# Optimization experiments

Hardware: AMD Instinct MI355X
Metric: run time of the kernel (lower is better)

The kernel has to match this reference:

```python
import jax, jax.numpy as jnp
import numpy as np

B = 2048          # args.batch_size
NPOS = 3          # n_positives
D = 128           # feature dim
TEMP = 0.1        # temperature
N_NEG = 4096      # args.n_negative
WEIGHT = 1.0      # args.multi_pos_weight
N = B * (1 + NPOS)  # total rows in z = 8192


def setup_inputs() -> dict:
    key = jax.random.key(0)
    k1, k2 = jax.random.split(key)
    return {
        "x": jax.random.normal(k1, (NPOS * B, D), dtype=jnp.float32),
        "x_pair": jax.random.normal(k2, (B, D), dtype=jnp.float32),
    }


def _l2n(a):
    return a / jnp.linalg.norm(a, axis=-1, keepdims=True)


def reference(x, x_pair):
    # z = cat(x, x_pair); full cosine-similarity matrix scaled by temperature
    z = jnp.concatenate([x, x_pair], axis=0)          # [N, D]
    zn = _l2n(z)
    sim = (zn @ zn.T) / TEMP                          # [N, N]

    # positive loss: per-row cosine(p, x_pair) for each of NPOS chunks of x
    xn = _l2n(x.reshape(NPOS, B, D))                  # [NPOS, B, D]
    pn = _l2n(x_pair)                                 # [B, D]
    pos = jnp.sum(xn * pn[None, :, :], axis=-1) / TEMP  # [NPOS, B]
    loss_pos = WEIGHT * pos.mean(axis=1).sum() / NPOS

    # drop diagonal: row i keeps all columns j != i (row-major, matches boolean-mask reshape)
    cols = jnp.arange(N - 1)[None, :]
    cols = cols + (cols >= jnp.arange(N)[:, None])    # [N, N-1]
    neg = jnp.take_along_axis(sim, cols, axis=1)      # [N, N-1]

    # random negative subsampling: per-row random permutation, keep first N_NEG
    u = jax.random.uniform(jax.random.key(42), (N, N - 1))
    perm = jnp.argsort(u, axis=1)[:, :N_NEG]          # [N, N_NEG]
    neg = jnp.take_along_axis(neg, perm, axis=1)

    loss_neg = jax.nn.logsumexp(neg, axis=1).mean()
    return loss_neg - loss_pos
```

## Files before the change

kernel.cpp:

```cpp
#include <hip/hip_runtime.h>
#include <hip/hip_bf16.h>
#include <stdint.h>

#define NTOT 8192
#define DD   128
#define BB   2048
#define NX   6144
#define LOG_SUB_FRAC (-0.6930251f)
#define SQRT10 3.16227766017f

typedef __attribute__((ext_vector_type(4))) float floatx4;

#define GLOBAL_AS(p) ((const __attribute__((address_space(1))) void*)(p))
#define LDS_AS(p)    ((__attribute__((address_space(3))) void*)(p))

template <int CTRL>
__device__ __forceinline__ float dpp_add(float s) {
  return s + __int_as_float(
      __builtin_amdgcn_update_dpp(0, __float_as_int(s), CTRL, 0xF, 0xF, true));
}
__device__ __forceinline__ float row16_sum(float s) {
  s = dpp_add<0xB1>(s);
  s = dpp_add<0x4E>(s);
  s = dpp_add<0x124>(s);
  s = dpp_add<0x128>(s);
  return s;
}

__global__ __launch_bounds__(256) void mp_norm(const float* __restrict__ x,
                                               const float* __restrict__ xp,
                                               uint8_t* __restrict__ znb8,
                                               float* __restrict__ pos,
                                               float* __restrict__ rowtotals) {
  const int z = blockIdx.x * 256 + threadIdx.x;
  if (z < NTOT) rowtotals[z] = 0.f;

  const int row  = blockIdx.x * 4 + (threadIdx.x >> 6);
  const int lane = threadIdx.x & 63;
  const bool isx = row < NX;
  const float* src = isx ? (x + (size_t)row * DD) : (xp + (size_t)(row - NX) * DD);
  float2 v = ((const float2*)src)[lane];
  float ss = v.x * v.x + v.y * v.y;

  float ssp = 0.f, d = 0.f;
  if (isx) {
    const int b = row & (BB - 1);
    float2 p = ((const float2*)(xp + (size_t)b * DD))[lane];
    ssp = p.x * p.x + p.y * p.y;
    d = v.x * p.x + v.y * p.y;
  }
  ss  = row16_sum(ss);  ss  += __shfl_xor(ss, 16, 64);  ss  += __shfl_xor(ss, 32, 64);
  if (isx) {
    ssp = row16_sum(ssp); ssp += __shfl_xor(ssp, 16, 64); ssp += __shfl_xor(ssp, 32, 64);
    d   = row16_sum(d);   d   += __shfl_xor(d, 16, 64);   d   += __shfl_xor(d, 32, 64);
  }
  const float rn = rsqrtf(ss);
  const float rns = rn * SQRT10;
  const int pk = __builtin_amdgcn_cvt_pk_fp8_f32(v.x * rns, v.y * rns, 0, false);
  *(uint16_t*)(znb8 + (size_t)row * DD + lane * 2) = (uint16_t)(pk & 0xffff);
  if (isx && lane == 0) pos[row] = d * rn * rsqrtf(ssp);
}

__global__ __launch_bounds__(256, 4) void mp_simexp(const uint8_t* __restrict__ znb8,
                                                    float* __restrict__ rowtotals) {
  __shared__ uint8_t Asmem[128 * 128];
  __shared__ uint8_t Bsmem[128 * 128];

  const int t = blockIdx.x;
  int bi = (int)((129.0f - sqrtf(16641.0f - 8.0f * (float)t)) * 0.5f);
  #define FCUM(r) ((r) * 64 - ((r) * ((r) - 1)) / 2)
  while (bi > 0 && FCUM(bi) > t) --bi;
  while (FCUM(bi + 1) <= t) ++bi;
  const int bj = bi + (t - FCUM(bi));
  const bool diag = (bi == bj);

  const int tid  = threadIdx.x;
  const int wave = tid >> 6, lane = tid & 63;
  const int lhi = lane >> 4, llo = lane & 15;

  const uint8_t* gA = znb8 + (size_t)bi * 128 * DD;
  const uint8_t* gB = znb8 + (size_t)bj * 128 * DD;

  #pragma unroll
  for (int tc = 0; tc < 4; ++tc) {
    const int c = wave * 4 + tc;
    const int row = c * 8 + (lane >> 3);
    const int p = (lane & 7) ^ (row & 7);
    const int roff = row * DD + p * 16;
    __builtin_amdgcn_global_load_lds(GLOBAL_AS(gA + roff), LDS_AS(&Asmem[c * 1024]), 16, 0, 0);
    if (!diag)
      __builtin_amdgcn_global_load_lds(GLOBAL_AS(gB + roff), LDS_AS(&Bsmem[c * 1024]), 16, 0, 0);
  }
  __syncthreads();
  const uint8_t* Bs = diag ? Asmem : Bsmem;

  const int wr = wave >> 1, wc = wave & 1;
  floatx4 acc[4][4] = {};
  #pragma unroll
  for (int kk = 0; kk < 4; ++kk) {
    const int c8 = kk * 4 + lhi;
    const int ph = c8 >> 1, hh = (c8 & 1) * 8;
    long a[4], b[4];
    #pragma unroll
    for (int r = 0; r < 4; ++r) {
      const int row = wr * 64 + r * 16 + llo;
      a[r] = *(const long*)&Asmem[row * DD + ((ph ^ (row & 7)) << 4) + hh];
    }
    #pragma unroll
    for (int c = 0; c < 4; ++c) {
      const int row = wc * 64 + c * 16 + llo;
      b[c] = *(const long*)&Bs[row * DD + ((ph ^ (row & 7)) << 4) + hh];
    }
    #pragma unroll
    for (int r = 0; r < 4; ++r)
      #pragma unroll
      for (int c = 0; c < 4; ++c)
        acc[r][c] = __builtin_amdgcn_mfma_f32_16x16x32_fp8_fp8(a[r], b[c], acc[r][c], 0, 0, 0);
  }

  float rowacc[4][4];
  #pragma unroll
  for (int r = 0; r < 4; ++r)
    #pragma unroll
    for (int j = 0; j < 4; ++j) rowacc[r][j] = 0.f;
  float colacc[4] = {0.f, 0.f, 0.f, 0.f};

  if (diag) {
    #pragma unroll
    for (int r = 0; r < 4; ++r) {
      #pragma unroll
      for (int c = 0; c < 4; ++c) {
        const int col = wc * 64 + c * 16 + llo;
        #pragma unroll
        for (int j = 0; j < 4; ++j) {
          const int row = wr * 64 + r * 16 + lhi * 4 + j;
          float e = __expf(acc[r][c][j]);
          if (row == col) e = 0.f;
          rowacc[r][j] += e;
          colacc[c] += e;
        }
      }
    }
  } else {
    #pragma unroll
    for (int r = 0; r < 4; ++r) {
      #pragma unroll
      for (int c = 0; c < 4; ++c) {
        #pragma unroll
        for (int j = 0; j < 4; ++j) {
          float e = __expf(acc[r][c][j]);
          rowacc[r][j] += e;
          colacc[c] += e;
        }
      }
    }
  }

  float* rowdst = rowtotals + bi * 128 + wr * 64;
  #pragma unroll
  for (int r = 0; r < 4; ++r) {
    #pragma unroll
    for (int j = 0; j < 4; ++j) {
      float s = row16_sum(rowacc[r][j]);
      if (llo == j) atomicAdd(&rowdst[r * 16 + lhi * 4 + j], s);
    }
  }
  if (!diag) {
    float* coldst = rowtotals + bj * 128 + wc * 64;
    #pragma unroll
    for (int c = 0; c < 4; ++c) {
      float s = colacc[c];
      s += __shfl_xor(s, 16, 64);
      s += __shfl_xor(s, 32, 64);
      if (lhi == 0) atomicAdd(&coldst[c * 16 + llo], s);
    }
  }
}

__global__ __launch_bounds__(1024) void mp_tail(const float* __restrict__ rowtotals,
                                                const float* __restrict__ pos,
                                                float* __restrict__ out) {
  const int tid = threadIdx.x;
  float l = 0.f;
  #pragma unroll
  for (int k = 0; k < 8; ++k) l += logf(rowtotals[k * 1024 + tid]);
  float p = 0.f;
  for (int t = tid; t < NX; t += 1024) p += pos[t];
  #pragma unroll
  for (int m = 1; m < 64; m <<= 1) {
    l += __shfl_xor(l, m, 64);
    p += __shfl_xor(p, m, 64);
  }
  __shared__ float rl[16], rp[16];
  if ((tid & 63) == 0) { rl[tid >> 6] = l; rp[tid >> 6] = p; }
  __syncthreads();
  if (tid == 0) {
    float S = 0.f, P = 0.f;
    #pragma unroll
    for (int w = 0; w < 16; ++w) { S += rl[w]; P += rp[w]; }
    const float loss_neg = S / (float)NTOT + LOG_SUB_FRAC;
    const float loss_pos = P * (10.0f / (float)NX);
    out[0] = loss_neg - loss_pos;
  }
}

extern "C" void kernel_launch(void* const* d_in, const int* in_sizes, int n_in,
                              void* d_out, int out_size, void* d_ws, size_t ws_size,
                              hipStream_t stream) {
  const float* x  = (const float*)d_in[0];
  const float* xp = (const float*)d_in[1];
  float* out = (float*)d_out;

  char* ws = (char*)d_ws;
  uint8_t* znb8    = (uint8_t*)ws;
  float* pos       = (float*)(ws + (1u << 20));
  float* rowtotals = (float*)(ws + (1u << 20) + (32u << 10));

  mp_norm<<<NTOT / 4, 256, 0, stream>>>(x, xp, znb8, pos, rowtotals);
  mp_simexp<<<2080, 256, 0, stream>>>(znb8, rowtotals);
  mp_tail<<<1, 1024, 0, stream>>>(rowtotals, pos, out);
}
```

Measured before the change: 92.83 us.

## Fuse tail reduction into simexp via last-block counter; use K=128 scaled FP8 MFMA

New measurement: 197.8 us. 2.13x slower.

```diff
diff --git a/kernel.cpp b/kernel.cpp
--- a/kernel.cpp
+++ b/kernel.cpp
@@ -8,8 +8,11 @@
 #define NX   6144
 #define LOG_SUB_FRAC (-0.6930251f)
 #define SQRT10 3.16227766017f
+#define NBLK 2080
 
 typedef __attribute__((ext_vector_type(4))) float floatx4;
+typedef __attribute__((ext_vector_type(4))) int   intx4;
+typedef __attribute__((ext_vector_type(8))) int   intx8;
 
 #define GLOBAL_AS(p) ((const __attribute__((address_space(1))) void*)(p))
 #define LDS_AS(p)    ((__attribute__((address_space(3))) void*)(p))
@@ -31,9 +34,11 @@
                                                const float* __restrict__ xp,
                                                uint8_t* __restrict__ znb8,
                                                float* __restrict__ pos,
-                                               float* __restrict__ rowtotals) {
+                                               float* __restrict__ rowtotals,
+                                               unsigned int* __restrict__ donecnt) {
   const int z = blockIdx.x * 256 + threadIdx.x;
   if (z < NTOT) rowtotals[z] = 0.f;
+  if (z == 0) donecnt[0] = 0u;
 
   const int row  = blockIdx.x * 4 + (threadIdx.x >> 6);
   const int lane = threadIdx.x & 63;
@@ -62,7 +67,10 @@
 }
 
 __global__ __launch_bounds__(256, 4) void mp_simexp(const uint8_t* __restrict__ znb8,
-                                                    float* __restrict__ rowtotals) {
+                                                    const float* __restrict__ pos,
+                                                    float* __restrict__ rowtotals,
+                                                    unsigned int* __restrict__ donecnt,
+                                                    float* __restrict__ out) {
   __shared__ uint8_t Asmem[128 * 128];
   __shared__ uint8_t Bsmem[128 * 128];
 
@@ -96,26 +104,26 @@
 
   const int wr = wave >> 1, wc = wave & 1;
   floatx4 acc[4][4] = {};
-  #pragma unroll
-  for (int kk = 0; kk < 4; ++kk) {
-    const int c8 = kk * 4 + lhi;
-    const int ph = c8 >> 1, hh = (c8 & 1) * 8;
-    long a[4], b[4];
-    #pragma unroll
-    for (int r = 0; r < 4; ++r) {
-      const int row = wr * 64 + r * 16 + llo;
-      a[r] = *(const long*)&Asmem[row * DD + ((ph ^ (row & 7)) << 4) + hh];
-    }
-    #pragma unroll
-    for (int c = 0; c < 4; ++c) {
-      const int row = wc * 64 + c * 16 + llo;
-      b[c] = *(const long*)&Bs[row * DD + ((ph ^ (row & 7)) << 4) + hh];
-    }
-    #pragma unroll
-    for (int r = 0; r < 4; ++r)
-      #pragma unroll
-      for (int c = 0; c < 4; ++c)
-        acc[r][c] = __builtin_amdgcn_mfma_f32_16x16x32_fp8_fp8(a[r], b[c], acc[r][c], 0, 0, 0);
+  intx8 bfrag[4];
+  #pragma unroll
+  for (int c = 0; c < 4; ++c) {
+    const int row = wc * 64 + c * 16 + llo;
+    const uint8_t* base = Bs + row * DD;
+    intx4 lo = *(const intx4*)(base + (((2 * lhi)     ^ (row & 7)) << 4));
+    intx4 hi = *(const intx4*)(base + (((2 * lhi + 1) ^ (row & 7)) << 4));
+    bfrag[c] = intx8{lo.x, lo.y, lo.z, lo.w, hi.x, hi.y, hi.z, hi.w};
+  }
+  #pragma unroll
+  for (int r = 0; r < 4; ++r) {
+    const int row = wr * 64 + r * 16 + llo;
+    const uint8_t* base = Asmem + row * DD;
+    intx4 lo = *(const intx4*)(base + (((2 * lhi)     ^ (row & 7)) << 4));
+    intx4 hi = *(const intx4*)(base + (((2 * lhi + 1) ^ (row & 7)) << 4));
+    intx8 afrag = intx8{lo.x, lo.y, lo.z, lo.w, hi.x, hi.y, hi.z, hi.w};
+    #pragma unroll
+    for (int c = 0; c < 4; ++c)
+      acc[r][c] = __builtin_amdgcn_mfma_scale_f32_16x16x128_f8f6f4(
+          afrag, bfrag[c], acc[r][c], 0, 0, 0, 0x7F7F7F7F, 0, 0x7F7F7F7F);
   }
 
   float rowacc[4][4];
@@ -175,32 +183,35 @@
       if (lhi == 0) atomicAdd(&coldst[c * 16 + llo], s);
     }
   }
-}
-
-__global__ __launch_bounds__(1024) void mp_tail(const float* __restrict__ rowtotals,
-                                                const float* __restrict__ pos,
-                                                float* __restrict__ out) {
-  const int tid = threadIdx.x;
-  float l = 0.f;
-  #pragma unroll
-  for (int k = 0; k < 8; ++k) l += logf(rowtotals[k * 1024 + tid]);
-  float p = 0.f;
-  for (int t = tid; t < NX; t += 1024) p += pos[t];
-  #pragma unroll
-  for (int m = 1; m < 64; m <<= 1) {
-    l += __shfl_xor(l, m, 64);
-    p += __shfl_xor(p, m, 64);
-  }
-  __shared__ float rl[16], rp[16];
-  if ((tid & 63) == 0) { rl[tid >> 6] = l; rp[tid >> 6] = p; }
+
+  __threadfence();
+  __shared__ unsigned int lastFlag;
+  if (tid == 0) lastFlag = (atomicAdd(donecnt, 1u) == NBLK - 1) ? 1u : 0u;
   __syncthreads();
-  if (tid == 0) {
-    float S = 0.f, P = 0.f;
-    #pragma unroll
-    for (int w = 0; w < 16; ++w) { S += rl[w]; P += rp[w]; }
-    const float loss_neg = S / (float)NTOT + LOG_SUB_FRAC;
-    const float loss_pos = P * (10.0f / (float)NX);
-    out[0] = loss_neg - loss_pos;
+  if (lastFlag) {
+    __threadfence();
+    float l = 0.f;
+    #pragma unroll
+    for (int k = 0; k < 32; ++k)
+      l += logf(atomicAdd(&rowtotals[k * 256 + tid], 0.f));
+    float p = 0.f;
+    #pragma unroll
+    for (int k = 0; k < 24; ++k) p += pos[k * 256 + tid];
+    #pragma unroll
+    for (int m = 1; m < 64; m <<= 1) {
+      l += __shfl_xor(l, m, 64);
+      p += __shfl_xor(p, m, 64);
+    }
+    __shared__ float rl[4], rp[4];
+    if ((tid & 63) == 0) { rl[tid >> 6] = l; rp[tid >> 6] = p; }
+    __syncthreads();
+    if (tid == 0) {
+      const float S = rl[0] + rl[1] + rl[2] + rl[3];
+      const float P = rp[0] + rp[1] + rp[2] + rp[3];
+      const float loss_neg = S / (float)NTOT + LOG_SUB_FRAC;
+      const float loss_pos = P * (10.0f / (float)NX);
+      out[0] = loss_neg - loss_pos;
+    }
   }
 }
 
@@ -212,11 +223,11 @@
   float* out = (float*)d_out;
 
   char* ws = (char*)d_ws;
-  uint8_t* znb8    = (uint8_t*)ws;
-  float* pos       = (float*)(ws + (1u << 20));
-  float* rowtotals = (float*)(ws + (1u << 20) + (32u << 10));
-
-  mp_norm<<<NTOT / 4, 256, 0, stream>>>(x, xp, znb8, pos, rowtotals);
-  mp_simexp<<<2080, 256, 0, stream>>>(znb8, rowtotals);
-  mp_tail<<<1, 1024, 0, stream>>>(rowtotals, pos, out);
-}
+  uint8_t* znb8          = (uint8_t*)ws;
+  float* pos             = (float*)(ws + (1u << 20));
+  float* rowtotals       = (float*)(ws + (1u << 20) + (32u << 10));
+  unsigned int* donecnt  = (unsigned int*)(ws + (1u << 20) + (64u << 10));
+
+  mp_norm<<<NTOT / 4, 256, 0, stream>>>(x, xp, znb8, pos, rowtotals, donecnt);
+  mp_simexp<<<NBLK, 256, 0, stream>>>(znb8, pos, rowtotals, donecnt, out);
+}
```
